# Optimization experiments

Measured on AMD Instinct MI355X. Metric: run time of the kernel, lower is better.

The kernel has to match this reference:

```python
import jax, jax.numpy as jnp
import numpy as np

B, S, C, H = 256, 512, 64, 128  # batch, seq_len, input channels, LSTM hidden


def setup_inputs() -> dict:
    key = jax.random.key(0)
    ks = jax.random.split(key, 9)
    s = 1.0 / np.sqrt(H)  # torch nn.LSTM init: U(-1/sqrt(H), 1/sqrt(H))
    u = lambda k, shape: jax.random.uniform(k, shape, jnp.float32, -s, s)
    return {
        "x": jax.random.normal(ks[0], (B, S, C), jnp.float32),
        # layer 0 (input size C)
        "Wih0": u(ks[1], (4 * H, C)),
        "Whh0": u(ks[2], (4 * H, H)),
        "bih0": u(ks[3], (4 * H,)),
        "bhh0": u(ks[4], (4 * H,)),
        # layer 1 (input size H)
        "Wih1": u(ks[5], (4 * H, H)),
        "Whh1": u(ks[6], (4 * H, H)),
        "bih1": u(ks[7], (4 * H,)),
        "bhh1": u(ks[8], (4 * H,)),
    }


def _lstm_layer(x, Wih, Whh, bih, bhh):
    """x: (S, B, in) -> outputs h_t for all t: (S, B, H). Torch gate order i,f,g,o."""
    Hh = Whh.shape[1]
    # Input-to-hidden GEMM hoisted out of the recurrence (batched over S).
    xg = jnp.einsum('sbc,gc->sbg', x, Wih) + bih + bhh  # (S, B, 4H)

    def step(carry, xt):
        h, c = carry
        g = xt + h @ Whh.T  # (B, 4H)
        i, f, gg, o = jnp.split(g, 4, axis=-1)
        i = jax.nn.sigmoid(i)
        f = jax.nn.sigmoid(f)
        gg = jnp.tanh(gg)
        o = jax.nn.sigmoid(o)
        c = f * c + i * gg
        h = o * jnp.tanh(c)
        return (h, c), h

    h0 = jnp.zeros((x.shape[1], Hh), x.dtype)
    _, ys = jax.lax.scan(step, (h0, h0), xg)
    return ys


def reference(x, Wih0, Whh0, bih0, bhh0, Wih1, Whh1, bih1, bhh1):
    xs = jnp.transpose(x, (1, 0, 2))  # (B,S,C) -> (S,B,C), matching x.permute(1,0,2)
    y1 = _lstm_layer(xs, Wih0, Whh0, bih0, bhh0)
    y2 = _lstm_layer(y1, Wih1, Whh1, bih1, bhh1)
    return y2[-1]  # x[-1, :, :]: last timestep of top layer, (B, H)
```

## Files before the change

### kernel.cpp

```cpp
#include <hip/hip_runtime.h>
#include <cstdint>
#include <cstddef>


#define S_LEN 512
#define B_SZ  256
#define C_IN  64
#define HDIM  128
#define CH    16
#define NBLK  32

using short8  = __attribute__((ext_vector_type(8))) short;
using float4v = __attribute__((ext_vector_type(4))) float;

__device__ __forceinline__ unsigned short f2b(float f) {
    union { float f; unsigned int u; } v; v.f = f;
    unsigned int u = v.u;
    return (unsigned short)((u + 0x7FFFu + ((u >> 16) & 1u)) >> 16);
}
__device__ __forceinline__ float sig_(float x) {
    return __builtin_amdgcn_rcpf(1.0f + __builtin_amdgcn_exp2f(x * -1.442695041f));
}
__device__ __forceinline__ float tanh_(float x) {
    return 1.0f - 2.0f * __builtin_amdgcn_rcpf(1.0f + __builtin_amdgcn_exp2f(x * 2.885390082f));
}

__global__ void prep_kernel(const float* __restrict__ x,
                            const float* __restrict__ wih0, const float* __restrict__ whh0,
                            const float* __restrict__ bih0, const float* __restrict__ bhh0,
                            const float* __restrict__ wih1, const float* __restrict__ whh1,
                            const float* __restrict__ bih1, const float* __restrict__ bhh1,
                            unsigned short* __restrict__ whh0_b, unsigned short* __restrict__ wih0_b,
                            unsigned short* __restrict__ whh1_b, unsigned short* __restrict__ wih1_b,
                            float* __restrict__ bias0, float* __restrict__ bias1,
                            unsigned short* __restrict__ xb) {
    int i = blockIdx.x * blockDim.x + threadIdx.x;
    if (i < B_SZ * S_LEN * C_IN) xb[i] = f2b(x[i]);
    if (i < 4 * HDIM * HDIM) {
        whh0_b[i] = f2b(whh0[i]);
        whh1_b[i] = f2b(whh1[i]);
        wih1_b[i] = f2b(wih1[i]);
    }
    if (i < 4 * HDIM * C_IN) wih0_b[i] = f2b(wih0[i]);
    if (i < 4 * HDIM) {
        bias0[i] = bih0[i] + bhh0[i];
        bias1[i] = bih1[i] + bhh1[i];
    }
}

template<int KIN, bool IS_L0>
__device__ __forceinline__ void lstm_layer(
    unsigned short* hbuf,
    const unsigned short* __restrict__ in_seq,
    const unsigned short* __restrict__ wih_b,
    const unsigned short* __restrict__ whh_b,
    const float* __restrict__ bias,
    unsigned short* __restrict__ y1,
    float* __restrict__ final_out,
    int* __restrict__ flags, int blk) {
    constexpr int NKIN = KIN / 32;
    const int tid = threadIdx.x;
    const int w = tid >> 6, L = tid & 63, q = L >> 4, r = L & 15;
    const int boff = blk * 8, j0 = w * 16;
    const int rowload = (r >> 2) * 2 + (r & 1);

    short8 whh[4][4], wih[4][NKIN];
    float bias_s[4];
#pragma unroll
    for (int g = 0; g < 4; ++g) {
        const int nrow = g * HDIM + j0 + r;
#pragma unroll
        for (int kk = 0; kk < 4; ++kk)
            whh[g][kk] = *(const short8*)(whh_b + (size_t)nrow * HDIM + kk * 32 + q * 8);
#pragma unroll
        for (int kk = 0; kk < NKIN; ++kk)
            wih[g][kk] = *(const short8*)(wih_b + (size_t)nrow * KIN + kk * 32 + q * 8);
        bias_s[g] = bias[g * HDIM + j0 + r];
    }

    for (int idx = tid; idx < 2 * 2048; idx += 512) hbuf[idx] = 0;
    float cf[2] = {0.f, 0.f};

    const unsigned short* p;
    size_t stride;
    if constexpr (IS_L0) {
        p = in_seq + ((size_t)(boff + rowload) * S_LEN) * C_IN + q * 8;
        stride = C_IN;
    } else {
        p = in_seq + (size_t)(boff + rowload) * HDIM + q * 8;
        stride = (size_t)B_SZ * HDIM;
    }

    if constexpr (!IS_L0) {
        if (tid == 0)
            while (__hip_atomic_load(flags + blk * 32, __ATOMIC_ACQUIRE,
                                     __HIP_MEMORY_SCOPE_AGENT) != 1)
                __builtin_amdgcn_s_sleep(8);
    }
    __syncthreads();

    short8 xA[NKIN], xB[NKIN];
#pragma unroll
    for (int kk = 0; kk < NKIN; ++kk) xA[kk] = *(const short8*)(p + kk * 32);
    p += stride;

    const int cc = tid & 15, ii = (tid & 127) >> 4;
    const int mii = 4 * (ii >> 1) + (ii & 1);
    unsigned short* yst = y1 + (size_t)(boff + ii) * HDIM + cc * 8;

    const int j = j0 + r;
    const int chunkbase = (j >> 3) * 128 + (j & 7);
    float* fout = final_out ? final_out + (size_t)(boff + 2 * q) * HDIM + j : nullptr;

    auto step = [&](unsigned short* cur, unsigned short* nxt, short8* xc, short8* xn, int t) {
        short8 hfrag[4];
#pragma unroll
        for (int kk = 0; kk < 4; ++kk)
            hfrag[kk] = *(const short8*)(cur + ((kk * 4 + q) * 16 + r) * 8);

        if (t < S_LEN - 1) {
            if constexpr (!IS_L0) {
                if (((t + 1) & (CH - 1)) == 0) {
                    const int ch = (t + 1) / CH;
                    if (tid == 0)
                        while (__hip_atomic_load(flags + blk * 32 + ch, __ATOMIC_ACQUIRE,
                                                 __HIP_MEMORY_SCOPE_AGENT) != ch + 1)
                            __builtin_amdgcn_s_sleep(8);
                    __syncthreads();
                }
            }
#pragma unroll
            for (int kk = 0; kk < NKIN; ++kk) xn[kk] = *(const short8*)(p + kk * 32);
        }
        p += stride;

        float4v acc[4];
#pragma unroll
        for (int g = 0; g < 4; ++g) {
            float4v a = {bias_s[g], bias_s[g], bias_s[g], bias_s[g]};
#pragma unroll
            for (int kk = 0; kk < 4; ++kk)
                a = __builtin_amdgcn_mfma_f32_16x16x32_bf16(hfrag[kk], whh[g][kk], a, 0, 0, 0);
#pragma unroll
            for (int kk = 0; kk < NKIN; ++kk)
                a = __builtin_amdgcn_mfma_f32_16x16x32_bf16(xc[kk], wih[g][kk], a, 0, 0, 0);
            acc[g] = a;
        }

#pragma unroll
        for (int rr = 0; rr < 2; ++rr) {
            const float iv = sig_(acc[0][rr]);
            const float fv = sig_(acc[1][rr]);
            const float gv = tanh_(acc[2][rr]);
            const float ov = sig_(acc[3][rr]);
            cf[rr] = fv * cf[rr] + iv * gv;
            const float hv = ov * tanh_(cf[rr]);
            nxt[chunkbase + (4 * q + rr) * 8] = f2b(hv);
            if constexpr (!IS_L0) {
                if (t == S_LEN - 1) fout[rr * HDIM] = hv;
            }
        }
        __syncthreads();

        if constexpr (IS_L0) {
            if (tid < 128)
                *(short8*)yst = *(const short8*)(nxt + cc * 128 + mii * 8);
            yst += (size_t)B_SZ * HDIM;
            if ((t & (CH - 1)) == (CH - 1)) {
                __threadfence();
                __syncthreads();
                if (tid == 0) {
                    const int ch = t / CH;
                    __hip_atomic_store(flags + blk * 32 + ch, ch + 1, __ATOMIC_RELEASE,
                                       __HIP_MEMORY_SCOPE_AGENT);
                }
            }
        }
    };

    unsigned short* b0 = hbuf;
    unsigned short* b1 = hbuf + 2048;
    for (int t = 0; t < S_LEN; t += 2) {
        step(b0, b1, xA, xB, t);
        step(b1, b0, xB, xA, t + 1);
    }
}

__global__ __launch_bounds__(512, 2)
void lstm_pipe(const unsigned short* __restrict__ xb,
               const unsigned short* __restrict__ wih0_b, const unsigned short* __restrict__ whh0_b,
               const float* __restrict__ bias0,
               const unsigned short* __restrict__ wih1_b, const unsigned short* __restrict__ whh1_b,
               const float* __restrict__ bias1,
               unsigned short* __restrict__ y1, float* __restrict__ out,
               int* __restrict__ flags) {
    __shared__ __align__(16) unsigned short hbuf[2 * 2048];
    if (blockIdx.x < NBLK)
        lstm_layer<C_IN, true>(hbuf, xb, wih0_b, whh0_b, bias0, y1, nullptr, flags, blockIdx.x);
    else
        lstm_layer<HDIM, false>(hbuf, y1, wih1_b, whh1_b, bias1, nullptr, out, flags,
                                blockIdx.x - NBLK);
}


extern "C" void kernel_launch(void* const* d_in, const int* in_sizes, int n_in,
                              void* d_out, int out_size, void* d_ws, size_t ws_size,
                              hipStream_t stream) {
    const float* x    = (const float*)d_in[0];
    const float* wih0 = (const float*)d_in[1];
    const float* whh0 = (const float*)d_in[2];
    const float* bih0 = (const float*)d_in[3];
    const float* bhh0 = (const float*)d_in[4];
    const float* wih1 = (const float*)d_in[5];
    const float* whh1 = (const float*)d_in[6];
    const float* bih1 = (const float*)d_in[7];
    const float* bhh1 = (const float*)d_in[8];

    char* ws = (char*)d_ws;
    unsigned short* whh0_b = (unsigned short*)(ws + 0);
    unsigned short* wih0_b = (unsigned short*)(ws + 131072);
    unsigned short* whh1_b = (unsigned short*)(ws + 196608);
    unsigned short* wih1_b = (unsigned short*)(ws + 327680);
    float*          bias0  = (float*)(ws + 458752);
    float*          bias1  = (float*)(ws + 460800);
    int*            flags  = (int*)(ws + 462848);
    unsigned short* xb     = (unsigned short*)(ws + 524288);
    unsigned short* y1     = (unsigned short*)(ws + 17301504);

    hipMemsetAsync(flags, 0, 4096, stream);

    prep_kernel<<<(B_SZ * S_LEN * C_IN + 255) / 256, 256, 0, stream>>>(
        x, wih0, whh0, bih0, bhh0, wih1, whh1, bih1, bhh1,
        whh0_b, wih0_b, whh1_b, wih1_b, bias0, bias1, xb);

    lstm_pipe<<<dim3(2 * NBLK), dim3(512), 0, stream>>>(
        xb, wih0_b, whh0_b, bias0, wih1_b, whh1_b, bias1, y1, (float*)d_out, flags);
}
```

Measured before the change: 734.9 us.

## Split batch across twice as many blocks and hoist input projection out of the recurrence

The kernel now runs 64 block pairs, each owning 4 batch rows instead of 8, so twice as many CUs work on the recurrence. The input-to-hidden MFMAs are computed four timesteps at a time into an LDS buffer (xgf). Each recurrent step then only runs the Whh MFMAs, using four independent accumulator chains interleaved. This shortens the serial dependency chain per timestep. The costs are extra LDS traffic, poorly filled MFMA tiles (only 4 of 16 batch rows are used), more flag memory, and a larger flag-polling footprint.

```diff
diff --git a/kernel.cpp b/kernel.cpp
--- a/kernel.cpp
+++ b/kernel.cpp
@@ -8,7 +8,7 @@
 #define C_IN  64
 #define HDIM  128
 #define CH    16
-#define NBLK  32
+#define NPAIR 64
 
 using short8  = __attribute__((ext_vector_type(8))) short;
 using float4v = __attribute__((ext_vector_type(4))) float;
@@ -51,6 +51,7 @@
 template<int KIN, bool IS_L0>
 __device__ __forceinline__ void lstm_layer(
     unsigned short* hbuf,
+    float* xgf,
     const unsigned short* __restrict__ in_seq,
     const unsigned short* __restrict__ wih_b,
     const unsigned short* __restrict__ whh_b,
@@ -58,131 +59,115 @@
     unsigned short* __restrict__ y1,
     float* __restrict__ final_out,
     int* __restrict__ flags, int blk) {
-    constexpr int NKIN = KIN / 32;
+    constexpr int KK = KIN / 32;
     const int tid = threadIdx.x;
     const int w = tid >> 6, L = tid & 63, q = L >> 4, r = L & 15;
-    const int boff = blk * 8, j0 = w * 16;
-    const int rowload = (r >> 2) * 2 + (r & 1);
-
-    short8 whh[4][4], wih[4][NKIN];
+    const int boff = blk * 4, j0 = w * 16, j = j0 + r;
+
+    short8 whh[4][4], wih[4][KK];
     float bias_s[4];
 #pragma unroll
     for (int g = 0; g < 4; ++g) {
-        const int nrow = g * HDIM + j0 + r;
+        const int nrow = g * HDIM + j;
 #pragma unroll
         for (int kk = 0; kk < 4; ++kk)
             whh[g][kk] = *(const short8*)(whh_b + (size_t)nrow * HDIM + kk * 32 + q * 8);
 #pragma unroll
-        for (int kk = 0; kk < NKIN; ++kk)
+        for (int kk = 0; kk < KK; ++kk)
             wih[g][kk] = *(const short8*)(wih_b + (size_t)nrow * KIN + kk * 32 + q * 8);
-        bias_s[g] = bias[g * HDIM + j0 + r];
-    }
-
-    for (int idx = tid; idx < 2 * 2048; idx += 512) hbuf[idx] = 0;
-    float cf[2] = {0.f, 0.f};
-
-    const unsigned short* p;
-    size_t stride;
-    if constexpr (IS_L0) {
-        p = in_seq + ((size_t)(boff + rowload) * S_LEN) * C_IN + q * 8;
-        stride = C_IN;
-    } else {
-        p = in_seq + (size_t)(boff + rowload) * HDIM + q * 8;
-        stride = (size_t)B_SZ * HDIM;
-    }
-
-    if constexpr (!IS_L0) {
-        if (tid == 0)
-            while (__hip_atomic_load(flags + blk * 32, __ATOMIC_ACQUIRE,
-                                     __HIP_MEMORY_SCOPE_AGENT) != 1)
-                __builtin_amdgcn_s_sleep(8);
-    }
-    __syncthreads();
-
-    short8 xA[NKIN], xB[NKIN];
-#pragma unroll
-    for (int kk = 0; kk < NKIN; ++kk) xA[kk] = *(const short8*)(p + kk * 32);
-    p += stride;
-
-    const int cc = tid & 15, ii = (tid & 127) >> 4;
-    const int mii = 4 * (ii >> 1) + (ii & 1);
-    unsigned short* yst = y1 + (size_t)(boff + ii) * HDIM + cc * 8;
-
-    const int j = j0 + r;
-    const int chunkbase = (j >> 3) * 128 + (j & 7);
-    float* fout = final_out ? final_out + (size_t)(boff + 2 * q) * HDIM + j : nullptr;
-
-    auto step = [&](unsigned short* cur, unsigned short* nxt, short8* xc, short8* xn, int t) {
-        short8 hfrag[4];
-#pragma unroll
-        for (int kk = 0; kk < 4; ++kk)
-            hfrag[kk] = *(const short8*)(cur + ((kk * 4 + q) * 16 + r) * 8);
-
-        if (t < S_LEN - 1) {
-            if constexpr (!IS_L0) {
-                if (((t + 1) & (CH - 1)) == 0) {
-                    const int ch = (t + 1) / CH;
-                    if (tid == 0)
-                        while (__hip_atomic_load(flags + blk * 32 + ch, __ATOMIC_ACQUIRE,
-                                                 __HIP_MEMORY_SCOPE_AGENT) != ch + 1)
-                            __builtin_amdgcn_s_sleep(8);
-                    __syncthreads();
+        bias_s[g] = bias[g * HDIM + j];
+    }
+
+    for (int idx = tid; idx < 4096; idx += 512) hbuf[idx] = 0;
+    float cf = 0.f;
+
+    short8 af[KK];
+    auto loadA = [&](int ch, int sub) {
+        const int t = ch * CH + sub * 4 + (r >> 2);
+        const int b = boff + (r & 3);
+        const unsigned short* base;
+        if constexpr (IS_L0) base = in_seq + ((size_t)b * S_LEN + t) * C_IN;
+        else                 base = in_seq + ((size_t)t * B_SZ + b) * HDIM;
+#pragma unroll
+        for (int kk = 0; kk < KK; ++kk)
+            af[kk] = *(const short8*)(base + kk * 32 + q * 8);
+    };
+
+    if constexpr (IS_L0) loadA(0, 0);
+
+    for (int ch = 0; ch < 32; ++ch) {
+        if constexpr (!IS_L0) {
+            if (tid == 0)
+                while (__hip_atomic_load(flags + blk * 32 + ch, __ATOMIC_ACQUIRE,
+                                         __HIP_MEMORY_SCOPE_AGENT) != ch + 1)
+                    __builtin_amdgcn_s_sleep(2);
+            __syncthreads();
+            loadA(ch, 0);
+        }
+#pragma unroll 1
+        for (int sub = 0; sub < 4; ++sub) {
+#pragma unroll
+            for (int g = 0; g < 4; ++g) {
+                float4v a = {0.f, 0.f, 0.f, 0.f};
+#pragma unroll
+                for (int kk = 0; kk < KK; ++kk)
+                    a = __builtin_amdgcn_mfma_f32_16x16x32_bf16(af[kk], wih[g][kk], a, 0, 0, 0);
+#pragma unroll
+                for (int rr = 0; rr < 4; ++rr)
+                    xgf[((q * 8 + w) * 64 + rr * 16 + r) * 4 + g] = a[rr] + bias_s[g];
+            }
+            if (sub < 3) loadA(ch, sub + 1);
+            else if (IS_L0 && ch < 31) loadA(ch + 1, 0);
+            __syncthreads();
+
+#pragma unroll
+            for (int sl = 0; sl < 4; ++sl) {
+                const int s = sub * 4 + sl;
+                const int t = ch * CH + s;
+                unsigned short* cur = hbuf + (s & 1) * 2048;
+                unsigned short* nxt = hbuf + ((s & 1) ^ 1) * 2048;
+                short8 hfrag[4];
+#pragma unroll
+                for (int kk = 0; kk < 4; ++kk)
+                    hfrag[kk] = *(const short8*)(cur + ((kk * 4 + q) * 16 + r) * 8);
+                const float4v xv = ((const float4v*)xgf)[(sl * 8 + w) * 64 + L];
+                float4v a0 = {xv[0], 0.f, 0.f, 0.f};
+                float4v a1 = {xv[1], 0.f, 0.f, 0.f};
+                float4v a2 = {xv[2], 0.f, 0.f, 0.f};
+                float4v a3 = {xv[3], 0.f, 0.f, 0.f};
+#pragma unroll
+                for (int kk = 0; kk < 4; ++kk) {
+                    a0 = __builtin_amdgcn_mfma_f32_16x16x32_bf16(hfrag[kk], whh[0][kk], a0, 0, 0, 0);
+                    a1 = __builtin_amdgcn_mfma_f32_16x16x32_bf16(hfrag[kk], whh[1][kk], a1, 0, 0, 0);
+                    a2 = __builtin_amdgcn_mfma_f32_16x16x32_bf16(hfrag[kk], whh[2][kk], a2, 0, 0, 0);
+                    a3 = __builtin_amdgcn_mfma_f32_16x16x32_bf16(hfrag[kk], whh[3][kk], a3, 0, 0, 0);
                 }
-            }
-#pragma unroll
-            for (int kk = 0; kk < NKIN; ++kk) xn[kk] = *(const short8*)(p + kk * 32);
-        }
-        p += stride;
-
-        float4v acc[4];
-#pragma unroll
-        for (int g = 0; g < 4; ++g) {
-            float4v a = {bias_s[g], bias_s[g], bias_s[g], bias_s[g]};
-#pragma unroll
-            for (int kk = 0; kk < 4; ++kk)
-                a = __builtin_amdgcn_mfma_f32_16x16x32_bf16(hfrag[kk], whh[g][kk], a, 0, 0, 0);
-#pragma unroll
-            for (int kk = 0; kk < NKIN; ++kk)
-                a = __builtin_amdgcn_mfma_f32_16x16x32_bf16(xc[kk], wih[g][kk], a, 0, 0, 0);
-            acc[g] = a;
-        }
-
-#pragma unroll
-        for (int rr = 0; rr < 2; ++rr) {
-            const float iv = sig_(acc[0][rr]);
-            const float fv = sig_(acc[1][rr]);
-            const float gv = tanh_(acc[2][rr]);
-            const float ov = sig_(acc[3][rr]);
-            cf[rr] = fv * cf[rr] + iv * gv;
-            const float hv = ov * tanh_(cf[rr]);
-            nxt[chunkbase + (4 * q + rr) * 8] = f2b(hv);
-            if constexpr (!IS_L0) {
-                if (t == S_LEN - 1) fout[rr * HDIM] = hv;
-            }
-        }
-        __syncthreads();
-
-        if constexpr (IS_L0) {
-            if (tid < 128)
-                *(short8*)yst = *(const short8*)(nxt + cc * 128 + mii * 8);
-            yst += (size_t)B_SZ * HDIM;
-            if ((t & (CH - 1)) == (CH - 1)) {
-                __threadfence();
+                const float iv = sig_(a0[0]);
+                const float fv = sig_(a1[0]);
+                const float gv = tanh_(a2[0]);
+                const float ov = sig_(a3[0]);
+                cf = fv * cf + iv * gv;
+                const float hv = ov * tanh_(cf);
+                nxt[(j >> 3) * 128 + 32 * q + (j & 7)] = f2b(hv);
+                if constexpr (!IS_L0) {
+                    if (t == S_LEN - 1)
+                        final_out[(size_t)(boff + q) * HDIM + j] = hv;
+                }
                 __syncthreads();
-                if (tid == 0) {
-                    const int ch = t / CH;
-                    __hip_atomic_store(flags + blk * 32 + ch, ch + 1, __ATOMIC_RELEASE,
-                                       __HIP_MEMORY_SCOPE_AGENT);
+                if constexpr (IS_L0) {
+                    if (tid < 64)
+                        *(short8*)(y1 + ((size_t)t * B_SZ + boff + (L >> 4)) * HDIM + (L & 15) * 8)
+                            = *(const short8*)(nxt + (L & 15) * 128 + (L >> 4) * 32);
                 }
             }
         }
-    };
-
-    unsigned short* b0 = hbuf;
-    unsigned short* b1 = hbuf + 2048;
-    for (int t = 0; t < S_LEN; t += 2) {
-        step(b0, b1, xA, xB, t);
-        step(b1, b0, xB, xA, t + 1);
+        if constexpr (IS_L0) {
+            __threadfence();
+            __syncthreads();
+            if (tid == 0)
+                __hip_atomic_store(flags + blk * 32 + ch, ch + 1, __ATOMIC_RELEASE,
+                                   __HIP_MEMORY_SCOPE_AGENT);
+        }
     }
 }
 
@@ -195,11 +180,13 @@
                unsigned short* __restrict__ y1, float* __restrict__ out,
                int* __restrict__ flags) {
     __shared__ __align__(16) unsigned short hbuf[2 * 2048];
-    if (blockIdx.x < NBLK)
-        lstm_layer<C_IN, true>(hbuf, xb, wih0_b, whh0_b, bias0, y1, nullptr, flags, blockIdx.x);
+    __shared__ __align__(16) float xgf[4 * 8 * 64 * 4];
+    if (blockIdx.x < NPAIR)
+        lstm_layer<C_IN, true>(hbuf, xgf, xb, wih0_b, whh0_b, bias0, y1, nullptr,
+                               flags, blockIdx.x);
     else
-        lstm_layer<HDIM, false>(hbuf, y1, wih1_b, whh1_b, bias1, nullptr, out, flags,
-                                blockIdx.x - NBLK);
+        lstm_layer<HDIM, false>(hbuf, xgf, y1, wih1_b, whh1_b, bias1, nullptr, out,
+                                flags, blockIdx.x - NPAIR);
 }
 
 
@@ -227,12 +214,12 @@
     unsigned short* xb     = (unsigned short*)(ws + 524288);
     unsigned short* y1     = (unsigned short*)(ws + 17301504);
 
-    hipMemsetAsync(flags, 0, 4096, stream);
+    hipMemsetAsync(flags, 0, 8192, stream);
 
     prep_kernel<<<(B_SZ * S_LEN * C_IN + 255) / 256, 256, 0, stream>>>(
         x, wih0, whh0, bih0, bhh0, wih1, whh1, bih1, bhh1,
         whh0_b, wih0_b, whh1_b, wih1_b, bias0, bias1, xb);
 
-    lstm_pipe<<<dim3(2 * NBLK), dim3(512), 0, stream>>>(
+    lstm_pipe<<<dim3(2 * NPAIR), dim3(512), 0, stream>>>(
         xb, wih0_b, whh0_b, bias0, wih1_b, whh1_b, bias1, y1, (float*)d_out, flags);
 }
```

Measured after the change: 784.4 us. 6.7% more time.
